# Kernel tuning notes

Measured on AMD Instinct MI355X. Metric: run time of the kernel, lower is better.

The kernel has to match this reference:

```python
import jax, jax.numpy as jnp
import numpy as np

B, T, F, H, OUT, L = 4096, 336, 12, 50, 1, 3


def _lstm_layer(x_tbf, W_ih, W_hh, b_ih, b_hh):
    """PyTorch-semantics LSTM layer. x_tbf: [T,B,in]; returns [T,B,H]."""
    Hh = W_hh.shape[1]
    Bsz = x_tbf.shape[1]
    # precompute input projection for all timesteps: [T,B,4H]
    xz = jnp.einsum('tbf,gf->tbg', x_tbf, W_ih) + (b_ih + b_hh)

    def step(carry, xz_t):
        h, c = carry
        z = xz_t + h @ W_hh.T  # [B,4H]
        i, f, g, o = jnp.split(z, 4, axis=-1)  # PyTorch gate order i,f,g,o
        c = jax.nn.sigmoid(f) * c + jax.nn.sigmoid(i) * jnp.tanh(g)
        h = jax.nn.sigmoid(o) * jnp.tanh(c)
        return (h, c), h

    h0 = jnp.zeros((Bsz, Hh), x_tbf.dtype)
    c0 = jnp.zeros((Bsz, Hh), x_tbf.dtype)
    _, hs = jax.lax.scan(step, (h0, c0), xz)
    return hs


def setup_inputs() -> dict:
    key = jax.random.key(0)
    ks = jax.random.split(key, 16)
    s = 1.0 / np.sqrt(H)  # PyTorch LSTM init scale
    inp = {"x": jax.random.normal(ks[0], (B, T, F), dtype=jnp.float32)}
    in_sizes = [F, H, H]
    k = 1
    for l in range(L):
        inp[f"W_ih_{l}"] = jax.random.uniform(ks[k], (4 * H, in_sizes[l]), jnp.float32, -s, s); k += 1
        inp[f"W_hh_{l}"] = jax.random.uniform(ks[k], (4 * H, H), jnp.float32, -s, s); k += 1
        inp[f"b_ih_{l}"] = jax.random.uniform(ks[k], (4 * H,), jnp.float32, -s, s); k += 1
        inp[f"b_hh_{l}"] = jax.random.uniform(ks[k], (4 * H,), jnp.float32, -s, s); k += 1
    inp["W_lin"] = jax.random.uniform(ks[13], (OUT, H), jnp.float32, -s, s)
    inp["b_lin"] = jax.random.uniform(ks[14], (OUT,), jnp.float32, -s, s)
    return inp


def reference(x, W_ih_0, W_hh_0, b_ih_0, b_hh_0,
              W_ih_1, W_hh_1, b_ih_1, b_hh_1,
              W_ih_2, W_hh_2, b_ih_2, b_hh_2,
              W_lin, b_lin):
    h = jnp.transpose(x, (1, 0, 2))  # [T,B,F] time-major for scan
    params = [(W_ih_0, W_hh_0, b_ih_0, b_hh_0),
              (W_ih_1, W_hh_1, b_ih_1, b_hh_1),
              (W_ih_2, W_hh_2, b_ih_2, b_hh_2)]
    for W_ih, W_hh, bi, bh in params:
        h = _lstm_layer(h, W_ih, W_hh, bi, bh)  # [T,B,H]
    last = h[-1]  # out[:, -1, :] in batch_first layout
    return last @ W_lin.T + b_lin  # [B,OUT]
```

## Files before the change

### kernel.cpp

```cpp
#include <hip/hip_runtime.h>


#define Bsz 4096
#define Tt  336
#define BT  16
#define NTH 1024

typedef _Float16 half8 __attribute__((ext_vector_type(8)));
typedef float    floatx4 __attribute__((ext_vector_type(4)));

struct __align__(16) SMem {
  _Float16 act0[2][BT * 64];
  _Float16 act1[2][BT * 128];
  _Float16 act2[2][BT * 128];
};

__device__ __forceinline__ int offA0(int n, int L) {
  return n * 64 + ((((L >> 3) ^ n) & 7) << 3) + (L & 7);
}
__device__ __forceinline__ int offA12(int n, int L) {
  return n * 128 + ((((L >> 3) ^ n) & 15) << 3) + (L & 7);
}

__device__ __forceinline__ float lstm_cell(floatx4 z, float& c) {
  float ei = __builtin_amdgcn_exp2f(z[0]);
  float ef = __builtin_amdgcn_exp2f(z[1]);
  float eg = __builtin_amdgcn_exp2f(z[2]);
  float eo = __builtin_amdgcn_exp2f(z[3]);
  float ig = __builtin_amdgcn_rcpf(1.f + ei);
  float fg = __builtin_amdgcn_rcpf(1.f + ef);
  float rg = __builtin_amdgcn_rcpf(1.f + eg);
  float og = __builtin_amdgcn_rcpf(1.f + eo);
  float gg = 1.f - 2.f * rg;
  c = fg * c + ig * gg;
  float ec = __builtin_amdgcn_exp2f(2.885390082f * c);
  float rc = __builtin_amdgcn_rcpf(1.f + ec);
  return og * (1.f - 2.f * rc);
}

__device__ __forceinline__ half8 wfrag(const float* __restrict__ Wih,
                                       const float* __restrict__ Whh,
                                       int lenih, int bound, int R, int k0) {
  half8 r = {};
  int u = R >> 2, g = R & 3;
  float sc = (g == 2) ? 2.885390082f : -1.442695041f;
  if (u < 50) {
    int row = g * 50 + u;
#pragma unroll
    for (int j = 0; j < 8; ++j) {
      int k = k0 + j;
      float v = 0.f;
      if (k < bound)           v = Wih[row * lenih + k];
      else if (k < bound + 50) v = Whh[row * 50 + (k - bound)];
      r[j] = (_Float16)(sc * v);
    }
  }
  return r;
}

#define MFMA(a, b, acc) __builtin_amdgcn_mfma_f32_16x16x32_f16((a), (b), (acc), 0, 0, 0)

__global__ __launch_bounds__(NTH, 4)
void lstm_mfma_kernel(const float* __restrict__ x,
                      const float* __restrict__ Wih0, const float* __restrict__ Whh0,
                      const float* __restrict__ bih0, const float* __restrict__ bhh0,
                      const float* __restrict__ Wih1, const float* __restrict__ Whh1,
                      const float* __restrict__ bih1, const float* __restrict__ bhh1,
                      const float* __restrict__ Wih2, const float* __restrict__ Whh2,
                      const float* __restrict__ bih2, const float* __restrict__ bhh2,
                      const float* __restrict__ Wlin, const float* __restrict__ blin,
                      float* __restrict__ out) {
  __shared__ SMem sm;
  const int tid  = threadIdx.x;
  const int blk  = blockIdx.x;
  const int lane = tid & 63;
  const int w    = tid >> 6;
  const int n    = lane & 15;
  const int q    = lane >> 4;

  {
    int* zp = (int*)&sm;
    for (int i = tid; i < (int)(sizeof(SMem) / 4); i += NTH) zp[i] = 0;
  }

  int Lw, nc, mm3[3] = {0, 0, 0};
  switch (w) {
    case 0:  Lw = 0; nc = 3; mm3[0] = 0;  mm3[1] = 1;  mm3[2] = 2;  break;
    case 1:  Lw = 0; nc = 2; mm3[0] = 3;  mm3[1] = 4;               break;
    case 2:  Lw = 0; nc = 3; mm3[0] = 5;  mm3[1] = 6;  mm3[2] = 7;  break;
    case 3:  Lw = 0; nc = 2; mm3[0] = 8;  mm3[1] = 9;               break;
    case 4:  Lw = 1; nc = 2; mm3[0] = 0;  mm3[1] = 1;               break;
    case 5:  Lw = 1; nc = 3; mm3[0] = 2;  mm3[1] = 3;  mm3[2] = 4;  break;
    case 6:  Lw = 1; nc = 2; mm3[0] = 5;  mm3[1] = 6;               break;
    case 7:  Lw = 1; nc = 3; mm3[0] = 7;  mm3[1] = 8;  mm3[2] = 9;  break;
    case 8:  Lw = 2; nc = 3; mm3[0] = 0;  mm3[1] = 1;  mm3[2] = 2;  break;
    case 9:  Lw = 2; nc = 2; mm3[0] = 3;  mm3[1] = 4;               break;
    case 10: Lw = 2; nc = 2; mm3[0] = 5;  mm3[1] = 6;               break;
    case 11: Lw = 2; nc = 2; mm3[0] = 7;  mm3[1] = 8;               break;
    case 12: Lw = 2; nc = 2; mm3[0] = 9;  mm3[1] = 10;              break;
    case 13: Lw = 0; nc = 3; mm3[0] = 10; mm3[1] = 11; mm3[2] = 12; break;
    case 14: Lw = 1; nc = 3; mm3[0] = 10; mm3[1] = 11; mm3[2] = 12; break;
    default: Lw = 2; nc = 2; mm3[0] = 11; mm3[1] = 12;              break;
  }
  const float* Wih = (Lw == 0) ? Wih0 : ((Lw == 1) ? Wih1 : Wih2);
  const float* Whh = (Lw == 0) ? Whh0 : ((Lw == 1) ? Whh1 : Whh2);
  const float* bih = (Lw == 0) ? bih0 : ((Lw == 1) ? bih1 : bih2);
  const float* bhh = (Lw == 0) ? bhh0 : ((Lw == 1) ? bhh1 : bhh2);

  half8  af[3][4];
  floatx4 bia[3];
  float  cst[3] = {0.f, 0.f, 0.f};
  int    woA[3], woB[3];
  bool   uokk[3];
#pragma unroll
  for (int i = 0; i < 3; ++i) {
    bia[i] = (floatx4){0, 0, 0, 0};
#pragma unroll
    for (int kc = 0; kc < 4; ++kc) af[i][kc] = (half8){};
    int m = mm3[i];
    int u = 4 * m + q;
    int uc = (u < 50) ? u : 49;
    uokk[i] = (i < nc) && (u < 50);
    if (Lw == 0) { woA[i] = offA0 (n, 12 + uc); woB[i] = offA12(n, 64 + uc); }
    else         { woA[i] = offA12(n, uc);      woB[i] = offA12(n, 64 + uc); }
    if (i < nc) {
      int R = 16 * m + n;
      if (Lw == 0) {
#pragma unroll
        for (int kc = 0; kc < 2; ++kc)
          af[i][kc] = wfrag(Wih, Whh, 12, 12, R, kc * 32 + q * 8);
      } else {
#pragma unroll
        for (int kc = 0; kc < 2; ++kc) {
          af[i][kc]     = wfrag(Whh, Whh, 50, 50, R, kc * 32 + q * 8);
          af[i][kc + 2] = wfrag(Wih, Whh, 50, 50, R, kc * 32 + q * 8);
        }
      }
      if (u < 50) {
#pragma unroll
        for (int g = 0; g < 4; ++g) {
          float sc = (g == 2) ? 2.885390082f : -1.442695041f;
          bia[i][g] = sc * (bih[g * 50 + u] + bhh[g * 50 + u]);
        }
      }
    }
  }

  const int ro0[2] = { offA0(n, q * 8), offA0(n, 32 + q * 8) };
  const int ro1[4] = { offA12(n, q * 8),      offA12(n, 32 + q * 8),
                       offA12(n, 64 + q * 8), offA12(n, 96 + q * 8) };

  half8 bpf[2][2] = {};

  const int sr = (tid < 192) ? tid / 12 : 0;
  const int sf = (tid < 192) ? tid - sr * 12 : 0;
  const int sxo = offA0(sr, sf);
  const float* xp = x + ((size_t)(blk * BT + sr) * Tt) * 12 + sf;
  float xnext = 0.f;

  __syncthreads();
  if (tid < 192) {
    sm.act0[0][sxo] = (_Float16)xp[0];
    xnext = xp[12];
  }
  __syncthreads();

#define TICK(p, TAU, CHK)                                                  \
  {                                                                        \
    if (Lw == 0) {                                                         \
      if (!(CHK) || (TAU) <= 335) {                                        \
        half8 b0 = *(const half8*)&sm.act0[p][ro0[0]];                     \
        half8 b1 = *(const half8*)&sm.act0[p][ro0[1]];                     \
        for (int i = 0; i < 3; ++i) if (i < nc) {                          \
          floatx4 z = bia[i];                                              \
          z = MFMA(af[i][0], b0, z);                                       \
          z = MFMA(af[i][1], b1, z);                                       \
          float h = lstm_cell(z, cst[i]);                                  \
          _Float16 hh = (_Float16)h;                                       \
          if (uokk[i]) { sm.act0[1 - (p)][woA[i]] = hh;                    \
                         sm.act1[1 - (p)][woB[i]] = hh; }                  \
        }                                                                  \
      }                                                                    \
    } else if (Lw == 1) {                                                  \
      half8 b0 = {}, b1 = {};                                              \
      if (!(CHK) || ((TAU) >= 2 && (TAU) <= 337)) {                        \
        b0 = *(const half8*)&sm.act1[p][ro1[0]];                           \
        b1 = *(const half8*)&sm.act1[p][ro1[1]];                           \
      }                                                                    \
      if (!(CHK) || ((TAU) >= 1 && (TAU) <= 336)) {                        \
        bpf[1 - (p)][0] = *(const half8*)&sm.act1[p][ro1[2]];              \
        bpf[1 - (p)][1] = *(const half8*)&sm.act1[p][ro1[3]];              \
      }                                                                    \
      if (!(CHK) || ((TAU) >= 2 && (TAU) <= 337)) {                        \
        for (int i = 0; i < 3; ++i) if (i < nc) {                          \
          floatx4 z = bia[i];                                              \
          z = MFMA(af[i][2], bpf[p][0], z);                                \
          z = MFMA(af[i][3], bpf[p][1], z);                                \
          z = MFMA(af[i][0], b0, z);                                       \
          z = MFMA(af[i][1], b1, z);                                       \
          float h = lstm_cell(z, cst[i]);                                  \
          _Float16 hh = (_Float16)h;                                       \
          if (uokk[i]) { sm.act1[1 - (p)][woA[i]] = hh;                    \
                         sm.act2[1 - (p)][woB[i]] = hh; }                  \
        }                                                                  \
      }                                                                    \
    } else {                                                               \
      half8 b0 = {}, b1 = {};                                              \
      if (!(CHK) || ((TAU) >= 4 && (TAU) <= 339)) {                        \
        b0 = *(const half8*)&sm.act2[p][ro1[0]];                           \
        b1 = *(const half8*)&sm.act2[p][ro1[1]];                           \
      }                                                                    \
      if (!(CHK) || ((TAU) >= 3 && (TAU) <= 338)) {                        \
        bpf[1 - (p)][0] = *(const half8*)&sm.act2[p][ro1[2]];              \
        bpf[1 - (p)][1] = *(const half8*)&sm.act2[p][ro1[3]];              \
      }                                                                    \
      if (!(CHK) || ((TAU) >= 4 && (TAU) <= 339)) {                        \
        for (int i = 0; i < 3; ++i) if (i < nc) {                          \
          floatx4 z = bia[i];                                              \
          z = MFMA(af[i][2], bpf[p][0], z);                                \
          z = MFMA(af[i][3], bpf[p][1], z);                                \
          z = MFMA(af[i][0], b0, z);                                       \
          z = MFMA(af[i][1], b1, z);                                       \
          float h = lstm_cell(z, cst[i]);                                  \
          if (uokk[i]) sm.act2[1 - (p)][woA[i]] = (_Float16)h;             \
        }                                                                  \
      }                                                                    \
    }                                                                      \
    if (tid < 192) {                                                       \
      if ((TAU) + 1 < Tt) sm.act0[1 - (p)][sxo] = (_Float16)xnext;         \
      xnext = ((TAU) + 2 < Tt) ? xp[((TAU) + 2) * 12] : 0.f;               \
    }                                                                      \
    __syncthreads();                                                       \
  }

  TICK(0, 0, 1)
  TICK(1, 1, 1)
  TICK(0, 2, 1)
  TICK(1, 3, 1)
#pragma unroll 1
  for (int t = 4; t < Tt; t += 2) {
    TICK(0, t, 0)
    TICK(1, t + 1, 0)
  }
  TICK(0, 336, 1)
  TICK(1, 337, 1)
  TICK(0, 338, 1)
  TICK(1, 339, 1)
#undef TICK

  if (tid < BT) {
    float s = blin[0];
    for (int uu = 0; uu < 50; ++uu)
      s += Wlin[uu] * (float)sm.act2[0][offA12(tid, uu)];
    out[blk * BT + tid] = s;
  }
}

extern "C" void kernel_launch(void* const* d_in, const int* in_sizes, int n_in,
                              void* d_out, int out_size, void* d_ws, size_t ws_size,
                              hipStream_t stream) {
  const float* x    = (const float*)d_in[0];
  const float* Wih0 = (const float*)d_in[1];
  const float* Whh0 = (const float*)d_in[2];
  const float* bih0 = (const float*)d_in[3];
  const float* bhh0 = (const float*)d_in[4];
  const float* Wih1 = (const float*)d_in[5];
  const float* Whh1 = (const float*)d_in[6];
  const float* bih1 = (const float*)d_in[7];
  const float* bhh1 = (const float*)d_in[8];
  const float* Wih2 = (const float*)d_in[9];
  const float* Whh2 = (const float*)d_in[10];
  const float* bih2 = (const float*)d_in[11];
  const float* bhh2 = (const float*)d_in[12];
  const float* Wlin = (const float*)d_in[13];
  const float* blin = (const float*)d_in[14];
  float* outp = (float*)d_out;

  dim3 grid(Bsz / BT);
  dim3 block(NTH);
  lstm_mfma_kernel<<<grid, block, 0, stream>>>(
      x, Wih0, Whh0, bih0, bhh0, Wih1, Whh1, bih1, bhh1,
      Wih2, Whh2, bih2, bhh2, Wlin, blin, outp);
}
```

Measured before the change: 394.7 us.

## Shrink per-layer activation buffers and interleave independent MFMA chains across cells

Each layer's hidden state is now written only once, into its own 64-wide buffer. The next layer reads its input from the previous layer's buffer instead of a duplicated upper half in a 128-wide buffer. This removes the second shared-memory store per cell, halves LDS use for layers 1 and 2, and rebuilds the weight fragments to match the new K ordering. The per-cell loop is also unrolled into explicit 2- or 3-way interleaved MFMA chains, so the independent accumulators hide MFMA latency before the gate math runs. The cost is more live registers and a branch on nc every tick.

```diff
diff --git a/kernel.cpp b/kernel.cpp
--- a/kernel.cpp
+++ b/kernel.cpp
@@ -11,15 +11,12 @@
 
 struct __align__(16) SMem {
   _Float16 act0[2][BT * 64];
-  _Float16 act1[2][BT * 128];
-  _Float16 act2[2][BT * 128];
+  _Float16 act1[2][BT * 64];
+  _Float16 act2[2][BT * 64];
 };
 
-__device__ __forceinline__ int offA0(int n, int L) {
+__device__ __forceinline__ int offA(int n, int L) {
   return n * 64 + ((((L >> 3) ^ n) & 7) << 3) + (L & 7);
-}
-__device__ __forceinline__ int offA12(int n, int L) {
-  return n * 128 + ((((L >> 3) ^ n) & 15) << 3) + (L & 7);
 }
 
 __device__ __forceinline__ float lstm_cell(floatx4 z, float& c) {
@@ -38,9 +35,9 @@
   return og * (1.f - 2.f * rc);
 }
 
-__device__ __forceinline__ half8 wfrag(const float* __restrict__ Wih,
-                                       const float* __restrict__ Whh,
-                                       int lenih, int bound, int R, int k0) {
+__device__ __forceinline__ half8 wfrag2(const float* __restrict__ Wa, int lena,
+                                        const float* __restrict__ Wb, int offb,
+                                        int lenb, int R, int k0) {
   half8 r = {};
   int u = R >> 2, g = R & 3;
   float sc = (g == 2) ? 2.885390082f : -1.442695041f;
@@ -50,8 +47,8 @@
     for (int j = 0; j < 8; ++j) {
       int k = k0 + j;
       float v = 0.f;
-      if (k < bound)           v = Wih[row * lenih + k];
-      else if (k < bound + 50) v = Whh[row * 50 + (k - bound)];
+      if (Wa && k < lena)                         v = Wa[row * lena + k];
+      else if (Wb && k >= offb && k < offb + lenb) v = Wb[row * lenb + (k - offb)];
       r[j] = (_Float16)(sc * v);
     }
   }
@@ -59,6 +56,50 @@
 }
 
 #define MFMA(a, b, acc) __builtin_amdgcn_mfma_f32_16x16x32_f16((a), (b), (acc), 0, 0, 0)
+
+#define CELLS(NCC, b0, b1, sw)                                          \
+  {                                                                     \
+    floatx4 z0 = bia[0], z1 = bia[1], z2 = bia[2];                      \
+    z0 = MFMA(af[0][0], b0, z0);                                        \
+    z1 = MFMA(af[1][0], b0, z1);                                        \
+    if (NCC == 3) z2 = MFMA(af[2][0], b0, z2);                          \
+    z0 = MFMA(af[0][1], b1, z0);                                        \
+    z1 = MFMA(af[1][1], b1, z1);                                        \
+    if (NCC == 3) z2 = MFMA(af[2][1], b1, z2);                          \
+    float h0v = lstm_cell(z0, cst[0]);                                  \
+    float h1v = lstm_cell(z1, cst[1]);                                  \
+    if (uokk[0]) (sw)[wo[0]] = (_Float16)h0v;                           \
+    if (uokk[1]) (sw)[wo[1]] = (_Float16)h1v;                           \
+    if (NCC == 3) {                                                     \
+      float h2v = lstm_cell(z2, cst[2]);                                \
+      if (uokk[2]) (sw)[wo[2]] = (_Float16)h2v;                         \
+    }                                                                   \
+  }
+
+#define CELLSD(NCC, b0, b1, pp, sw)                                     \
+  {                                                                     \
+    floatx4 z0 = bia[0], z1 = bia[1], z2 = bia[2];                      \
+    z0 = MFMA(af[0][2], bpf[pp][0], z0);                                \
+    z1 = MFMA(af[1][2], bpf[pp][0], z1);                                \
+    if (NCC == 3) z2 = MFMA(af[2][2], bpf[pp][0], z2);                  \
+    z0 = MFMA(af[0][3], bpf[pp][1], z0);                                \
+    z1 = MFMA(af[1][3], bpf[pp][1], z1);                                \
+    if (NCC == 3) z2 = MFMA(af[2][3], bpf[pp][1], z2);                  \
+    z0 = MFMA(af[0][0], b0, z0);                                        \
+    z1 = MFMA(af[1][0], b0, z1);                                        \
+    if (NCC == 3) z2 = MFMA(af[2][0], b0, z2);                          \
+    z0 = MFMA(af[0][1], b1, z0);                                        \
+    z1 = MFMA(af[1][1], b1, z1);                                        \
+    if (NCC == 3) z2 = MFMA(af[2][1], b1, z2);                          \
+    float h0v = lstm_cell(z0, cst[0]);                                  \
+    float h1v = lstm_cell(z1, cst[1]);                                  \
+    if (uokk[0]) (sw)[wo[0]] = (_Float16)h0v;                           \
+    if (uokk[1]) (sw)[wo[1]] = (_Float16)h1v;                           \
+    if (NCC == 3) {                                                     \
+      float h2v = lstm_cell(z2, cst[2]);                                \
+      if (uokk[2]) (sw)[wo[2]] = (_Float16)h2v;                         \
+    }                                                                   \
+  }
 
 __global__ __launch_bounds__(NTH, 4)
 void lstm_mfma_kernel(const float* __restrict__ x,
@@ -110,7 +151,7 @@
   half8  af[3][4];
   floatx4 bia[3];
   float  cst[3] = {0.f, 0.f, 0.f};
-  int    woA[3], woB[3];
+  int    wo[3];
   bool   uokk[3];
 #pragma unroll
   for (int i = 0; i < 3; ++i) {
@@ -121,19 +162,20 @@
     int u = 4 * m + q;
     int uc = (u < 50) ? u : 49;
     uokk[i] = (i < nc) && (u < 50);
-    if (Lw == 0) { woA[i] = offA0 (n, 12 + uc); woB[i] = offA12(n, 64 + uc); }
-    else         { woA[i] = offA12(n, uc);      woB[i] = offA12(n, 64 + uc); }
+    wo[i] = (Lw == 0) ? offA(n, 12 + uc) : offA(n, uc);
     if (i < nc) {
       int R = 16 * m + n;
       if (Lw == 0) {
 #pragma unroll
         for (int kc = 0; kc < 2; ++kc)
-          af[i][kc] = wfrag(Wih, Whh, 12, 12, R, kc * 32 + q * 8);
+          af[i][kc] = wfrag2(Wih, 12, Whh, 12, 50, R, kc * 32 + q * 8);
       } else {
 #pragma unroll
         for (int kc = 0; kc < 2; ++kc) {
-          af[i][kc]     = wfrag(Whh, Whh, 50, 50, R, kc * 32 + q * 8);
-          af[i][kc + 2] = wfrag(Wih, Whh, 50, 50, R, kc * 32 + q * 8);
+          af[i][kc] = wfrag2(Whh, 50, nullptr, 0, 0, R, kc * 32 + q * 8);
+          af[i][kc + 2] = (Lw == 1)
+              ? wfrag2(nullptr, 0, Wih, 12, 50, R, kc * 32 + q * 8)
+              : wfrag2(Wih, 50, nullptr, 0, 0, R, kc * 32 + q * 8);
         }
       }
       if (u < 50) {
@@ -146,15 +188,13 @@
     }
   }
 
-  const int ro0[2] = { offA0(n, q * 8), offA0(n, 32 + q * 8) };
-  const int ro1[4] = { offA12(n, q * 8),      offA12(n, 32 + q * 8),
-                       offA12(n, 64 + q * 8), offA12(n, 96 + q * 8) };
+  const int ro[2] = { offA(n, q * 8), offA(n, 32 + q * 8) };
 
   half8 bpf[2][2] = {};
 
   const int sr = (tid < 192) ? tid / 12 : 0;
   const int sf = (tid < 192) ? tid - sr * 12 : 0;
-  const int sxo = offA0(sr, sf);
+  const int sxo = offA(sr, sf);
   const float* xp = x + ((size_t)(blk * BT + sr) * Tt) * 12 + sf;
   float xnext = 0.f;
 
@@ -169,61 +209,38 @@
   {                                                                        \
     if (Lw == 0) {                                                         \
       if (!(CHK) || (TAU) <= 335) {                                        \
-        half8 b0 = *(const half8*)&sm.act0[p][ro0[0]];                     \
-        half8 b1 = *(const half8*)&sm.act0[p][ro0[1]];                     \
-        for (int i = 0; i < 3; ++i) if (i < nc) {                          \
-          floatx4 z = bia[i];                                              \
-          z = MFMA(af[i][0], b0, z);                                       \
-          z = MFMA(af[i][1], b1, z);                                       \
-          float h = lstm_cell(z, cst[i]);                                  \
-          _Float16 hh = (_Float16)h;                                       \
-          if (uokk[i]) { sm.act0[1 - (p)][woA[i]] = hh;                    \
-                         sm.act1[1 - (p)][woB[i]] = hh; }                  \
-        }                                                                  \
+        half8 b0 = *(const half8*)&sm.act0[p][ro[0]];                      \
+        half8 b1 = *(const half8*)&sm.act0[p][ro[1]];                      \
+        _Float16* sw = &sm.act0[1 - (p)][0];                               \
+        if (nc == 3) CELLS(3, b0, b1, sw) else CELLS(2, b0, b1, sw)        \
       }                                                                    \
     } else if (Lw == 1) {                                                  \
       half8 b0 = {}, b1 = {};                                              \
       if (!(CHK) || ((TAU) >= 2 && (TAU) <= 337)) {                        \
-        b0 = *(const half8*)&sm.act1[p][ro1[0]];                           \
-        b1 = *(const half8*)&sm.act1[p][ro1[1]];                           \
+        b0 = *(const half8*)&sm.act1[p][ro[0]];                            \
+        b1 = *(const half8*)&sm.act1[p][ro[1]];                            \
       }                                                                    \
       if (!(CHK) || ((TAU) >= 1 && (TAU) <= 336)) {                        \
-        bpf[1 - (p)][0] = *(const half8*)&sm.act1[p][ro1[2]];              \
-        bpf[1 - (p)][1] = *(const half8*)&sm.act1[p][ro1[3]];              \
+        bpf[1 - (p)][0] = *(const half8*)&sm.act0[p][ro[0]];               \
+        bpf[1 - (p)][1] = *(const half8*)&sm.act0[p][ro[1]];               \
       }                                                                    \
       if (!(CHK) || ((TAU) >= 2 && (TAU) <= 337)) {                        \
-        for (int i = 0; i < 3; ++i) if (i < nc) {                          \
-          floatx4 z = bia[i];                                              \
-          z = MFMA(af[i][2], bpf[p][0], z);                                \
-          z = MFMA(af[i][3], bpf[p][1], z);                                \
-          z = MFMA(af[i][0], b0, z);                                       \
-          z = MFMA(af[i][1], b1, z);                                       \
-          float h = lstm_cell(z, cst[i]);                                  \
-          _Float16 hh = (_Float16)h;                                       \
-          if (uokk[i]) { sm.act1[1 - (p)][woA[i]] = hh;                    \
-                         sm.act2[1 - (p)][woB[i]] = hh; }                  \
-        }                                                                  \
+        _Float16* sw = &sm.act1[1 - (p)][0];                               \
+        if (nc == 3) CELLSD(3, b0, b1, p, sw) else CELLSD(2, b0, b1, p, sw)\
       }                                                                    \
     } else {                                                               \
       half8 b0 = {}, b1 = {};                                              \
       if (!(CHK) || ((TAU) >= 4 && (TAU) <= 339)) {                        \
-        b0 = *(const half8*)&sm.act2[p][ro1[0]];                           \
-        b1 = *(const half8*)&sm.act2[p][ro1[1]];                           \
+        b0 = *(const half8*)&sm.act2[p][ro[0]];                            \
+        b1 = *(const half8*)&sm.act2[p][ro[1]];                            \
       }                                                                    \
       if (!(CHK) || ((TAU) >= 3 && (TAU) <= 338)) {                        \
-        bpf[1 - (p)][0] = *(const half8*)&sm.act2[p][ro1[2]];              \
-        bpf[1 - (p)][1] = *(const half8*)&sm.act2[p][ro1[3]];              \
+        bpf[1 - (p)][0] = *(const half8*)&sm.act1[p][ro[0]];               \
+        bpf[1 - (p)][1] = *(const half8*)&sm.act1[p][ro[1]];               \
       }                                                                    \
       if (!(CHK) || ((TAU) >= 4 && (TAU) <= 339)) {                        \
-        for (int i = 0; i < 3; ++i) if (i < nc) {                          \
-          floatx4 z = bia[i];                                              \
-          z = MFMA(af[i][2], bpf[p][0], z);                                \
-          z = MFMA(af[i][3], bpf[p][1], z);                                \
-          z = MFMA(af[i][0], b0, z);                                       \
-          z = MFMA(af[i][1], b1, z);                                       \
-          float h = lstm_cell(z, cst[i]);                                  \
-          if (uokk[i]) sm.act2[1 - (p)][woA[i]] = (_Float16)h;             \
-        }                                                                  \
+        _Float16* sw = &sm.act2[1 - (p)][0];                               \
+        if (nc == 3) CELLSD(3, b0, b1, p, sw) else CELLSD(2, b0, b1, p, sw)\
       }                                                                    \
     }                                                                      \
     if (tid < 192) {                                                       \
@@ -251,7 +268,7 @@
   if (tid < BT) {
     float s = blin[0];
     for (int uu = 0; uu < 50; ++uu)
-      s += Wlin[uu] * (float)sm.act2[0][offA12(tid, uu)];
+      s += Wlin[uu] * (float)sm.act2[0][offA(tid, uu)];
     out[blk * BT + tid] = s;
   }
 }
```

Result: no change. 394.3 us (-0.1%).
